# Optimization experiments

Hardware: AMD Instinct MI355X
Metric: run time of the kernel (lower is better)

The kernel has to match this reference:

```python
import jax, jax.numpy as jnp
import numpy as np

N = 1024      # total nodes in batch
H = 128       # node_dim == hid_dim
B = 128       # number of graphs
NPG = 8       # nodes per graph (<= MAX_NODES=9)
MAXN = 9
BT = 3        # bond_types
A = 3 * MAXN * MAXN  # action_space_length = 243


def setup_inputs() -> dict:
    key = jax.random.key(0)
    ks = jax.random.split(key, 8)
    node_features = jax.random.normal(ks[0], (N, H), jnp.float32) * 0.5
    seg = np.repeat(np.arange(B), NPG)  # contiguous graph membership (dgl batching)
    segment_ids = jnp.asarray(seg, jnp.int32)
    # len_vec[g, n] = 1 if node n belongs to graph g  ->  len_vec.T @ len_vec is the block-diagonal pair mask
    len_vec = jnp.asarray((seg[None, :] == np.arange(B)[:, None]).astype(np.float32))
    mask = jnp.zeros((B, A), jnp.float32)  # additive logit mask
    rng = np.random.default_rng(0)
    indexmask = jnp.asarray(np.argsort(rng.random((B, A)), axis=1).astype(np.int32))  # per-graph permutation of [0,243)
    batch_num_nodes = jnp.full((B,), NPG, jnp.int32)
    sc = lambda k, sh, fan: jax.random.normal(k, sh, jnp.float32) / np.sqrt(fan)
    W_fcv1 = sc(ks[1], (H, H // 2), H); b_fcv1 = jnp.zeros((H // 2,), jnp.float32)
    W_fcv2 = sc(ks[2], (H // 2, 1), H // 2); b_fcv2 = jnp.zeros((1,), jnp.float32)
    W_a2 = sc(ks[3], (2 * H, H), 2 * H); b_a2 = jnp.zeros((H,), jnp.float32)
    W_final = sc(ks[4], (H, BT), H); b_final = jnp.zeros((BT,), jnp.float32)
    return dict(node_features=node_features, len_vec=len_vec, mask=mask,
                W_fcv1=W_fcv1, b_fcv1=b_fcv1, W_fcv2=W_fcv2, b_fcv2=b_fcv2,
                W_a2=W_a2, b_a2=b_a2, W_final=W_final, b_final=b_final,
                indexmask=indexmask, segment_ids=segment_ids,
                batch_num_nodes=batch_num_nodes)


def reference(node_features, len_vec, mask, W_fcv1, b_fcv1, W_fcv2, b_fcv2,
              W_a2, b_a2, W_final, b_final, indexmask, segment_ids,
              batch_num_nodes):
    # --- value head: sum-pool per graph, relu(fcv1), fcv2 ---
    readout = jax.ops.segment_sum(node_features, segment_ids, num_segments=B)  # [B,H]
    readout = jax.nn.relu(readout @ W_fcv1 + b_fcv1) @ W_fcv2 + b_fcv2          # [B,1]

    # --- all-pairs features: cat([nf[i], nf[j]]) -> relu -> action_2 -> relu -> final ---
    # relu(cat(a,b)) = cat(relu(a),relu(b)); split W_a2 so we never materialize [N,N,2H]
    r = jax.nn.relu(node_features)          # [N,H]
    Ai = r @ W_a2[:H]                        # row-node (Y2) contribution  [N,H]
    Bj = r @ W_a2[H:]                        # col-node (X2) contribution  [N,H]
    hidden = jax.nn.relu(Ai[:, None, :] + Bj[None, :, :] + b_a2)   # [N,N,H]
    len_matrix = (len_vec.T @ len_vec)[..., None]                  # [N,N,1] block-diagonal 0/1
    scores = (jnp.einsum('ijh,hk->ijk', hidden, W_final) + b_final) * len_matrix  # [N,N,3]
    flat = scores.reshape(-1)

    # --- ragged per-graph gather of the nonzero (in-block) entries, padded to A=243 ---
    val = batch_num_nodes.astype(jnp.int32)          # [B]
    off = jnp.cumsum(val) - val                      # exclusive prefix (node offsets)
    s = jnp.arange(A, dtype=jnp.int32)[None, :]      # [1,A] slot index
    v = val[:, None]; o = off[:, None]
    i_loc = s // (v * BT)
    j_loc = (s % (v * BT)) // BT
    k = s % BT
    valid = s < v * v * BT                           # slots beyond val*val*3 are padding (-1 in torch code)
    flat_idx = ((o + i_loc) * N + (o + j_loc)) * BT + k
    flat_idx = jnp.clip(flat_idx, 0, N * N * BT - 1)
    gathered = jnp.where(valid, flat[flat_idx], jnp.float32(0.0))  # [B,A]

    # torch.index_select(final[idx], 0, indexmask[idx])
    fap = jnp.take_along_axis(gathered, indexmask.astype(jnp.int32), axis=1)
    probs = jax.nn.softmax(fap + mask, axis=1)
    return probs, readout
```

## Files before the change

### kernel.cpp

```cpp
#include <hip/hip_runtime.h>
#include <cfloat>

#define HH 128
#define BB 128
#define AA 243
#define MAXV 9

__device__ __forceinline__ float rl(float x, int l) {
    return __builtin_bit_cast(float, __builtin_amdgcn_readlane(__builtin_bit_cast(int, x), l));
}

__global__ __launch_bounds__(512) void apm_fused(
    const float* __restrict__ nf,
    const float* __restrict__ maskp,
    const float* __restrict__ W_fcv1,
    const float* __restrict__ b_fcv1,
    const float* __restrict__ W_fcv2,
    const float* __restrict__ b_fcv2,
    const float* __restrict__ W_a2,
    const float* __restrict__ b_a2,
    const float* __restrict__ W_final,
    const float* __restrict__ b_final,
    const int*   __restrict__ indexmask,
    const int*   __restrict__ bnn,
    float* __restrict__ probs_out,
    float* __restrict__ readout_out)
{
    const int b    = blockIdx.x;
    const int t    = threadIdx.x;
    const int lane = t & 63;
    const int w    = t >> 6;
    const int matB = w >> 2;
    const int hh   = (w >> 1) & 1;
    const int ch   = w & 1;
    const int c    = (ch << 6) | lane;

    __shared__ float pA[2][MAXV][132];
    __shared__ float pB[2][MAXV][132];
    __shared__ float wfT[3][HH];
    __shared__ float sc[AA + 1];
    __shared__ float rdbuf[HH];
    __shared__ float rout[64];
    __shared__ float xred[16];

    const float* Wb = W_a2 + matB * (HH * HH) + (hh * 64) * HH + c;
    float wreg[64];
    #pragma unroll
    for (int h = 0; h < 64; ++h) wreg[h] = Wb[h * HH];

    float mk = 0.f, bfin = 0.f; int im = 0;
    if (t < AA) {
        im   = indexmask[b * AA + t];
        mk   = maskp[b * AA + t];
        bfin = b_final[t % 3];
    }
    for (int idx = t; idx < 3 * HH; idx += 512) {
        int h = idx / 3, k = idx - 3 * h;
        wfT[k][h] = W_final[idx];
    }

    int ov = 0;
    if (lane < b)      ov += bnn[lane];
    if (lane + 64 < b) ov += bnn[lane + 64];
    #pragma unroll
    for (int o = 1; o < 64; o <<= 1) ov += __shfl_xor(ov, o, 64);
    const int off = ov;
    const int v   = bnn[b];

    float rr[MAXV]; float rdsum = 0.f;
    #pragma unroll
    for (int i = 0; i < MAXV; ++i) {
        float x = (i < v) ? nf[(off + i) * HH + hh * 64 + lane] : 0.f;
        rdsum += x;
        rr[i]  = fmaxf(x, 0.f);
    }
    if (w == 0) rdbuf[lane]      = rdsum;
    if (w == 2) rdbuf[64 + lane] = rdsum;

    float acc[MAXV];
    #pragma unroll
    for (int i = 0; i < MAXV; ++i) acc[i] = 0.f;
    #pragma unroll
    for (int h = 0; h < 64; ++h) {
        float wv = wreg[h];
        #pragma unroll
        for (int i = 0; i < MAXV; ++i) acc[i] = fmaf(rl(rr[i], h), wv, acc[i]);
    }
    {
        float (*dst)[132] = matB ? pB[hh] : pA[hh];
        #pragma unroll
        for (int i = 0; i < MAXV; ++i) dst[i][c] = acc[i];
    }
    __syncthreads();

    const int vv3 = v * v * 3;
    if (t < AA && t >= vv3) sc[t] = 0.f;

    float a2lo = 0.f;
    if (w < 6) {
        #pragma unroll
        for (int rep = 0; rep < 3; ++rep) {
            int idx = t + rep * 384;
            int i = idx >> 7, cc = idx & 127;
            pA[0][i][cc] = pA[0][i][cc] + pA[1][i][cc] + b_a2[cc];
            pB[0][i][cc] += pB[1][i][cc];
        }
    } else if (w == 6) {
        float rd1 = rdbuf[64 + lane];
        float a2 = 0.f;
        #pragma unroll
        for (int h = 0; h < 64; ++h)
            a2 = fmaf(rl(rd1, h), W_fcv1[(64 + h) * 64 + lane], a2);
        rout[lane] = a2;
    } else {
        float rd0 = rdbuf[lane];
        a2lo = b_fcv1[lane];
        #pragma unroll
        for (int h = 0; h < 64; ++h)
            a2lo = fmaf(rl(rd0, h), W_fcv1[h * 64 + lane], a2lo);
    }
    __syncthreads();

    if (t < vv3) {
        const int pair = t / 3, k = t - 3 * pair;
        const int i = pair / v, j = pair - i * v;
        const float* ar = &pA[0][i][0];
        const float* br = &pB[0][j][0];
        const float* wk = &wfT[k][0];
        float s = bfin;
        #pragma unroll 8
        for (int h = 0; h < HH; h += 4) {
            float4 a4 = *(const float4*)(ar + h);
            float4 b4 = *(const float4*)(br + h);
            float4 w4 = *(const float4*)(wk + h);
            s = fmaf(fmaxf(a4.x + b4.x, 0.f), w4.x, s);
            s = fmaf(fmaxf(a4.y + b4.y, 0.f), w4.y, s);
            s = fmaf(fmaxf(a4.z + b4.z, 0.f), w4.z, s);
            s = fmaf(fmaxf(a4.w + b4.w, 0.f), w4.w, s);
        }
        sc[t] = s;
    } else if (w == 7) {
        float a2 = a2lo + rout[lane];
        float x = fmaxf(a2, 0.f) * W_fcv2[lane];
        #pragma unroll
        for (int o = 1; o < 64; o <<= 1) x += __shfl_xor(x, o, 64);
        if (lane == 0) readout_out[b] = x + b_fcv2[0];
    }
    __syncthreads();

    float x = -FLT_MAX;
    if (t < AA) x = sc[im] + mk;
    float m = x;
    #pragma unroll
    for (int o = 1; o < 64; o <<= 1) m = fmaxf(m, __shfl_xor(m, o, 64));
    if (lane == 0) xred[w] = m;
    __syncthreads();
    m = fmaxf(fmaxf(xred[0], xred[1]), fmaxf(xred[2], xred[3]));
    float e = (t < AA) ? __expf(x - m) : 0.f;
    float s = e;
    #pragma unroll
    for (int o = 1; o < 64; o <<= 1) s += __shfl_xor(s, o, 64);
    if (lane == 0) xred[8 + w] = s;
    __syncthreads();
    const float denom = (xred[8] + xred[9]) + (xred[10] + xred[11]);
    const float rden  = __builtin_amdgcn_rcpf(denom);
    if (t < AA) probs_out[b * AA + t] = e * rden;
}

extern "C" void kernel_launch(void* const* d_in, const int* in_sizes, int n_in,
                              void* d_out, int out_size, void* d_ws, size_t ws_size,
                              hipStream_t stream) {
    const float* nf      = (const float*)d_in[0];
    const float* maskp   = (const float*)d_in[2];
    const float* W_fcv1  = (const float*)d_in[3];
    const float* b_fcv1  = (const float*)d_in[4];
    const float* W_fcv2  = (const float*)d_in[5];
    const float* b_fcv2  = (const float*)d_in[6];
    const float* W_a2    = (const float*)d_in[7];
    const float* b_a2    = (const float*)d_in[8];
    const float* W_final = (const float*)d_in[9];
    const float* b_final = (const float*)d_in[10];
    const int*   indexmask = (const int*)d_in[11];
    const int*   bnn       = (const int*)d_in[13];

    float* probs   = (float*)d_out;
    float* readout = probs + BB * AA;

    apm_fused<<<BB, 512, 0, stream>>>(nf, maskp, W_fcv1, b_fcv1, W_fcv2, b_fcv2,
                                      W_a2, b_a2, W_final, b_final,
                                      indexmask, bnn, probs, readout);
}
```

Baseline: 15.53 us.

## Split W_a2 projection into four h-quarters with float2 columns and break FMA chains

Each wave now handles a 32-row quarter of the hidden dimension and two output columns per lane (float2 weight loads), instead of a 64-row half and one column. The four partial sums are reduced through a larger shared buffer. The dependent FMA chains in the fcv1 and pair-score dot products are split into four independent accumulators to expose ILP, and the bnn loads are hoisted earlier to overlap with the weight loads. This costs more shared memory and a wider reduction step in exchange for shorter dependency chains and fewer readlanes per FMA.

```diff
diff --git a/kernel.cpp b/kernel.cpp
--- a/kernel.cpp
+++ b/kernel.cpp
@@ -31,22 +31,25 @@
     const int lane = t & 63;
     const int w    = t >> 6;
     const int matB = w >> 2;
-    const int hh   = (w >> 1) & 1;
-    const int ch   = w & 1;
-    const int c    = (ch << 6) | lane;
-
-    __shared__ float pA[2][MAXV][132];
-    __shared__ float pB[2][MAXV][132];
+    const int hq   = w & 3;
+    const int c0   = lane << 1;
+
+    __shared__ float pS[2][4][MAXV][132];
     __shared__ float wfT[3][HH];
     __shared__ float sc[AA + 1];
     __shared__ float rdbuf[HH];
     __shared__ float rout[64];
     __shared__ float xred[16];
 
-    const float* Wb = W_a2 + matB * (HH * HH) + (hh * 64) * HH + c;
-    float wreg[64];
-    #pragma unroll
-    for (int h = 0; h < 64; ++h) wreg[h] = Wb[h * HH];
+    int ov = 0;
+    if (lane < b)      ov += bnn[lane];
+    if (lane + 64 < b) ov += bnn[lane + 64];
+    const int v = bnn[b];
+
+    const float* Wb = W_a2 + matB * (HH * HH) + (hq * 32) * HH + c0;
+    float2 wreg[32];
+    #pragma unroll
+    for (int h = 0; h < 32; ++h) wreg[h] = *(const float2*)(Wb + h * HH);
 
     float mk = 0.f, bfin = 0.f; int im = 0;
     if (t < AA) {
@@ -54,43 +57,41 @@
         mk   = maskp[b * AA + t];
         bfin = b_final[t % 3];
     }
-    for (int idx = t; idx < 3 * HH; idx += 512) {
-        int h = idx / 3, k = idx - 3 * h;
-        wfT[k][h] = W_final[idx];
-    }
-
-    int ov = 0;
-    if (lane < b)      ov += bnn[lane];
-    if (lane + 64 < b) ov += bnn[lane + 64];
+    if (t < 3 * HH) {
+        int h = t / 3, k = t - 3 * h;
+        wfT[k][h] = W_final[t];
+    }
+
     #pragma unroll
     for (int o = 1; o < 64; o <<= 1) ov += __shfl_xor(ov, o, 64);
     const int off = ov;
-    const int v   = bnn[b];
-
+
+    const int hbase = hq * 32 + (lane & 31);
     float rr[MAXV]; float rdsum = 0.f;
     #pragma unroll
     for (int i = 0; i < MAXV; ++i) {
-        float x = (i < v) ? nf[(off + i) * HH + hh * 64 + lane] : 0.f;
+        float x = (i < v) ? nf[(off + i) * HH + hbase] : 0.f;
         rdsum += x;
         rr[i]  = fmaxf(x, 0.f);
     }
-    if (w == 0) rdbuf[lane]      = rdsum;
-    if (w == 2) rdbuf[64 + lane] = rdsum;
-
-    float acc[MAXV];
-    #pragma unroll
-    for (int i = 0; i < MAXV; ++i) acc[i] = 0.f;
-    #pragma unroll
-    for (int h = 0; h < 64; ++h) {
-        float wv = wreg[h];
-        #pragma unroll
-        for (int i = 0; i < MAXV; ++i) acc[i] = fmaf(rl(rr[i], h), wv, acc[i]);
-    }
-    {
-        float (*dst)[132] = matB ? pB[hh] : pA[hh];
-        #pragma unroll
-        for (int i = 0; i < MAXV; ++i) dst[i][c] = acc[i];
-    }
+    if (w < 4 && lane < 32) rdbuf[hbase] = rdsum;
+
+    float accx[MAXV], accy[MAXV];
+    #pragma unroll
+    for (int i = 0; i < MAXV; ++i) { accx[i] = 0.f; accy[i] = 0.f; }
+    #pragma unroll
+    for (int h = 0; h < 32; ++h) {
+        const float wx = wreg[h].x, wy = wreg[h].y;
+        #pragma unroll
+        for (int i = 0; i < MAXV; ++i) {
+            const float s = rl(rr[i], h);
+            accx[i] = fmaf(s, wx, accx[i]);
+            accy[i] = fmaf(s, wy, accy[i]);
+        }
+    }
+    #pragma unroll
+    for (int i = 0; i < MAXV; ++i)
+        *(float2*)&pS[matB][hq][i][c0] = make_float2(accx[i], accy[i]);
     __syncthreads();
 
     const int vv3 = v * v * 3;
@@ -101,44 +102,62 @@
         #pragma unroll
         for (int rep = 0; rep < 3; ++rep) {
             int idx = t + rep * 384;
-            int i = idx >> 7, cc = idx & 127;
-            pA[0][i][cc] = pA[0][i][cc] + pA[1][i][cc] + b_a2[cc];
-            pB[0][i][cc] += pB[1][i][cc];
+            int m   = idx / 576;
+            int rem = idx - m * 576;
+            int i   = rem >> 6;
+            int cc  = (rem & 63) << 1;
+            float2 p0 = *(const float2*)&pS[m][0][i][cc];
+            float2 p1 = *(const float2*)&pS[m][1][i][cc];
+            float2 p2 = *(const float2*)&pS[m][2][i][cc];
+            float2 p3 = *(const float2*)&pS[m][3][i][cc];
+            float sx = (p0.x + p1.x) + (p2.x + p3.x);
+            float sy = (p0.y + p1.y) + (p2.y + p3.y);
+            if (m == 0) { sx += b_a2[cc]; sy += b_a2[cc + 1]; }
+            *(float2*)&pS[m][0][i][cc] = make_float2(sx, sy);
         }
     } else if (w == 6) {
         float rd1 = rdbuf[64 + lane];
-        float a2 = 0.f;
-        #pragma unroll
-        for (int h = 0; h < 64; ++h)
-            a2 = fmaf(rl(rd1, h), W_fcv1[(64 + h) * 64 + lane], a2);
-        rout[lane] = a2;
+        float q0 = 0.f, q1 = 0.f, q2 = 0.f, q3 = 0.f;
+        #pragma unroll
+        for (int h = 0; h < 16; ++h) {
+            q0 = fmaf(rl(rd1, h),      W_fcv1[(64 + h)  * 64 + lane], q0);
+            q1 = fmaf(rl(rd1, h + 16), W_fcv1[(80 + h)  * 64 + lane], q1);
+            q2 = fmaf(rl(rd1, h + 32), W_fcv1[(96 + h)  * 64 + lane], q2);
+            q3 = fmaf(rl(rd1, h + 48), W_fcv1[(112 + h) * 64 + lane], q3);
+        }
+        rout[lane] = (q0 + q1) + (q2 + q3);
     } else {
         float rd0 = rdbuf[lane];
-        a2lo = b_fcv1[lane];
-        #pragma unroll
-        for (int h = 0; h < 64; ++h)
-            a2lo = fmaf(rl(rd0, h), W_fcv1[h * 64 + lane], a2lo);
+        float q0 = b_fcv1[lane], q1 = 0.f, q2 = 0.f, q3 = 0.f;
+        #pragma unroll
+        for (int h = 0; h < 16; ++h) {
+            q0 = fmaf(rl(rd0, h),      W_fcv1[h        * 64 + lane], q0);
+            q1 = fmaf(rl(rd0, h + 16), W_fcv1[(16 + h) * 64 + lane], q1);
+            q2 = fmaf(rl(rd0, h + 32), W_fcv1[(32 + h) * 64 + lane], q2);
+            q3 = fmaf(rl(rd0, h + 48), W_fcv1[(48 + h) * 64 + lane], q3);
+        }
+        a2lo = (q0 + q1) + (q2 + q3);
     }
     __syncthreads();
 
     if (t < vv3) {
         const int pair = t / 3, k = t - 3 * pair;
         const int i = pair / v, j = pair - i * v;
-        const float* ar = &pA[0][i][0];
-        const float* br = &pB[0][j][0];
+        const float* ar = &pS[0][0][i][0];
+        const float* br = &pS[1][0][j][0];
         const float* wk = &wfT[k][0];
-        float s = bfin;
+        float s0 = 0.f, s1 = 0.f, s2 = 0.f, s3 = 0.f;
         #pragma unroll 8
         for (int h = 0; h < HH; h += 4) {
             float4 a4 = *(const float4*)(ar + h);
             float4 b4 = *(const float4*)(br + h);
             float4 w4 = *(const float4*)(wk + h);
-            s = fmaf(fmaxf(a4.x + b4.x, 0.f), w4.x, s);
-            s = fmaf(fmaxf(a4.y + b4.y, 0.f), w4.y, s);
-            s = fmaf(fmaxf(a4.z + b4.z, 0.f), w4.z, s);
-            s = fmaf(fmaxf(a4.w + b4.w, 0.f), w4.w, s);
-        }
-        sc[t] = s;
+            s0 = fmaf(fmaxf(a4.x + b4.x, 0.f), w4.x, s0);
+            s1 = fmaf(fmaxf(a4.y + b4.y, 0.f), w4.y, s1);
+            s2 = fmaf(fmaxf(a4.z + b4.z, 0.f), w4.z, s2);
+            s3 = fmaf(fmaxf(a4.w + b4.w, 0.f), w4.w, s3);
+        }
+        sc[t] = bfin + ((s0 + s1) + (s2 + s3));
     } else if (w == 7) {
         float a2 = a2lo + rout[lane];
         float x = fmaxf(a2, 0.f) * W_fcv2[lane];
```

New measurement: 13.90 us. 10.4% less time.
